# Optimization experiments

Hardware: AMD Instinct MI355X
Metric: run time of the kernel (lower is better)

## Reference

```python
import jax, jax.numpy as jnp
import numpy as np
from jax import lax


def _nextpow2(v):
    return int(np.ceil(np.log2(abs(v))))


def _dct_matrix(N):
    # Orthonormal DCT-II matrix C: dct(x, norm='ortho') along last axis == x @ C.T
    # C is orthogonal, so idct(y, norm='ortho') == y @ C.
    n = jnp.arange(N, dtype=jnp.float32)
    k = n[:, None]
    C = 2.0 * jnp.cos(jnp.pi * (2.0 * n[None, :] + 1.0) * k / (2.0 * N))
    s = jnp.where(jnp.arange(N) == 0,
                  1.0 / jnp.sqrt(4.0 * N),
                  1.0 / jnp.sqrt(2.0 * N)).astype(jnp.float32)
    return s[:, None] * C


def setup_inputs() -> dict:
    key = jax.random.key(0)
    x = jax.random.normal(key, (2, 1, 128, 128), dtype=jnp.float32)
    tau = jnp.asarray(7.7e-11, dtype=jnp.float32)
    chi = jnp.asarray(0.03, dtype=jnp.float32)
    return {"x": x, "tau": tau, "chi": chi}


def _forward(x, c0=1.0, sigma=1.0):
    B, _, Nz, Nx = x.shape
    Lx = 2 ** (_nextpow2(2 * Nx) + 1)  # padded width (512 for Nx=128)
    Ly = 2 ** (_nextpow2(2 * Nz) + 1)  # padded height (512 for Nz=128)
    Cy = _dct_matrix(Ly)
    Cx = Cy if Lx == Ly else _dct_matrix(Lx)

    # np.block([[Z, W, ZP_col], [Z, Z, ZP_col], [ZP_row]]) places W at rows 0:Nz, cols Nx:2Nx
    P = jnp.zeros((B, Ly, Lx), x.dtype).at[:, 0:Nz, Nx:2 * Nx].set(x[:, 0])

    # 2D orthonormal DCT-II: P_hat = Cy @ P @ Cx.T
    P_hat = jnp.einsum('ki,bij,lj->bkl', Cy, P, Cx)

    # Only row 0 of the 2D IDCT is kept per timestep; row-0 of the axis-0 IDCT is
    # a fixed weighted sum with weights a[k] = Cy[k, 0].
    a = Cy[:, 0]
    M = a[None, :, None] * P_hat  # (B, Ly, Lx)

    kx = jnp.arange(Lx, dtype=jnp.float32) / Lx * jnp.pi
    ky = jnp.arange(Ly, dtype=jnp.float32) / Ly * jnp.pi
    F = jnp.sqrt(ky[:, None] ** 2 + kx[None, :] ** 2)  # f.T in the source: (Ly, Lx)

    def step(carry, t):
        phase = jnp.cos(c0 * F * t)                 # (Ly, Lx), shared over batch
        return carry, jnp.einsum('kj,bkj->bj', phase, M)

    _, V = lax.scan(step, None, jnp.arange(Ly, dtype=jnp.float32))  # (T, B, Lx)

    # Remaining IDCT along the last axis, then /3
    Pdet = jnp.transpose(V @ Cx, (1, 0, 2)) / 3.0   # (B, T=Ly, Lx)

    # additive noise: N(0, sigma * std(Pdet)) per batch element (np.std -> ddof=0)
    std = jnp.std(Pdet, axis=(1, 2), keepdims=True)
    noise = jax.random.normal(jax.random.key(42), Pdet.shape, Pdet.dtype) * (sigma * std)
    return (Pdet + noise)[:, None]                  # (B, 1, Ly, Lx)


def reference(x, tau, chi):
    # tau, chi are module parameters but unused in the original forward path
    return _forward(x)
```

## Files before the change

kernel.cpp:

```cpp
#include <hip/hip_runtime.h>
#include <stdint.h>
#include <math.h>


#define HALF_N 262144
#define PI_F 3.14159274101257324f


__device__ __forceinline__ uint32_t rotl32(uint32_t v, int r) {
  return (v << r) | (v >> (32 - r));
}

__device__ __forceinline__ float erfinv_xla(float x) {
  float w = -log1pf(__fmul_rn(-x, x));
  float p;
  if (w < 5.0f) {
    w = w - 2.5f;
    p = 2.81022636e-08f;
    p = fmaf(p, w, 3.43273939e-07f);
    p = fmaf(p, w, -3.5233877e-06f);
    p = fmaf(p, w, -4.39150654e-06f);
    p = fmaf(p, w, 0.00021858087f);
    p = fmaf(p, w, -0.00125372503f);
    p = fmaf(p, w, -0.00417768164f);
    p = fmaf(p, w, 0.246640727f);
    p = fmaf(p, w, 1.50140941f);
  } else {
    w = __fsqrt_rn(w) - 3.0f;
    p = -0.000200214257f;
    p = fmaf(p, w, 0.000100950558f);
    p = fmaf(p, w, 0.00134934322f);
    p = fmaf(p, w, -0.00367342844f);
    p = fmaf(p, w, 0.00573950773f);
    p = fmaf(p, w, -0.0076224613f);
    p = fmaf(p, w, 0.00943887047f);
    p = fmaf(p, w, 1.00167406f);
    p = fmaf(p, w, 2.83297682f);
  }
  return p * x;
}

__device__ __forceinline__ float cy_elem(float n2p1, float kf, float sc) {
  float t1 = __fmul_rn(PI_F, n2p1);
  float arg = __fmul_rn(t1, kf) * (1.0f / 1024.0f);
  return __fmul_rn(sc, __fmul_rn(2.0f, __cosf(arg)));
}

__global__ __launch_bounds__(512, 4) void stageB_kernel(const float* __restrict__ x,
                                                        float* __restrict__ Vt) {
  __shared__ float cyl[128];
  __shared__ float us[256];
  __shared__ float4 kq[512];
  __shared__ float red[8][512];
  int j = blockIdx.x;
  int tid = threadIdx.x;
  float jf = (float)j;
  if (tid < 128) {
    float scj = (j == 0) ? (1.0f / __fsqrt_rn(2048.0f)) : 0.03125f;
    cyl[tid] = cy_elem((float)(2 * (128 + tid) + 1), jf, scj);
  }
  __syncthreads();
  if (tid < 256) {
    int b = tid >> 7, i = tid & 127;
    const float* xr = x + (b * 128 + i) * 128;
    float accA = 0.0f, accB = 0.0f;
    for (int jj = 0; jj < 128; jj += 8) {
      float4 xa = *(const float4*)&xr[jj];
      float4 xb = *(const float4*)&xr[jj + 4];
      float4 ca = *(const float4*)&cyl[jj];
      float4 cb = *(const float4*)&cyl[jj + 4];
      accA = fmaf(xa.x, ca.x, accA); accB = fmaf(xa.y, ca.y, accB);
      accA = fmaf(xa.z, ca.z, accA); accB = fmaf(xa.w, ca.w, accB);
      accA = fmaf(xb.x, cb.x, accA); accB = fmaf(xb.y, cb.y, accB);
      accA = fmaf(xb.z, cb.z, accA); accB = fmaf(xb.w, cb.w, accB);
    }
    us[tid] = accA + accB;
  }
  __syncthreads();
  {
    float kf = (float)tid;
    float sc = (tid == 0) ? (1.0f / __fsqrt_rn(2048.0f)) : 0.03125f;
    float a = cy_elem(1.0f, kf, sc);
    float acc0 = __fmul_rn(a, us[0]);
    float acc1 = __fmul_rn(a, us[128]);
    float accA0 = 0.f, accA1 = 0.f;
    {
      float c1 = cy_elem(3.0f, kf, sc);
      float c2 = cy_elem(5.0f, kf, sc);
      float c3 = cy_elem(7.0f, kf, sc);
      acc0 = fmaf(c1, us[1], acc0);   acc1 = fmaf(c1, us[129], acc1);
      accA0 = fmaf(c2, us[2], accA0); accA1 = fmaf(c2, us[130], accA1);
      acc0 = fmaf(c3, us[3], acc0);   acc1 = fmaf(c3, us[131], acc1);
    }
    for (int i = 4; i < 128; i += 4) {
      float b0 = (float)(2 * i + 1);
      float c0 = cy_elem(b0, kf, sc);
      float c1 = cy_elem(__fadd_rn(b0, 2.0f), kf, sc);
      float c2 = cy_elem(__fadd_rn(b0, 4.0f), kf, sc);
      float c3 = cy_elem(__fadd_rn(b0, 6.0f), kf, sc);
      float4 u0 = *(const float4*)&us[i];
      float4 u1 = *(const float4*)&us[128 + i];
      acc0 = fmaf(c0, u0.x, acc0);   acc1 = fmaf(c0, u1.x, acc1);
      accA0 = fmaf(c1, u0.y, accA0); accA1 = fmaf(c1, u1.y, accA1);
      acc0 = fmaf(c2, u0.z, acc0);   acc1 = fmaf(c2, u1.z, acc1);
      accA0 = fmaf(c3, u0.w, accA0); accA1 = fmaf(c3, u1.w, accA1);
    }
    acc0 += accA0;
    acc1 += accA1;
    const float w0 = PI_F / 512.0f;
    float ky = __fmul_rn(kf, w0);
    float kx = __fmul_rn(jf, w0);
    float fsv = __fsqrt_rn(__fadd_rn(__fmul_rn(ky, ky), __fmul_rn(kx, kx)));
    float cs = __cosf(__fmul_rn(fsv, 64.0f));
    kq[tid] = make_float4(fsv, __fmul_rn(a, acc0), __fmul_rn(a, acc1), cs);
  }
  __syncthreads();
  int kg = tid >> 6, tg = tid & 63;
  int kbeg = kg << 6;
  float tfa = (float)tg;
  float tfb = (float)(tg + 64);
  float a0[8], a1[8];
#pragma unroll
  for (int n = 0; n < 8; ++n) { a0[n] = 0.0f; a1[n] = 0.0f; }
  for (int kk = 0; kk < 64; ++kk) {
    float4 q = kq[kbeg + kk];
    float F = q.x, m0 = q.y, m1 = q.z;
    float k2 = q.w + q.w;
    float ca = __cosf(__fmul_rn(F, tfa));
    float cb = __cosf(__fmul_rn(F, tfb));
    a0[0] = fmaf(ca, m0, a0[0]); a1[0] = fmaf(ca, m1, a1[0]);
    a0[1] = fmaf(cb, m0, a0[1]); a1[1] = fmaf(cb, m1, a1[1]);
#pragma unroll
    for (int n = 2; n < 8; ++n) {
      float cn = fmaf(k2, cb, -ca);
      a0[n] = fmaf(cn, m0, a0[n]); a1[n] = fmaf(cn, m1, a1[n]);
      ca = cb; cb = cn;
    }
  }
#pragma unroll
  for (int n = 0; n < 8; ++n) red[kg][(n << 6) + tg] = a0[n];
  __syncthreads();
  float s0 = red[0][tid];
#pragma unroll
  for (int g = 1; g < 8; ++g) s0 += red[g][tid];
  __syncthreads();
#pragma unroll
  for (int n = 0; n < 8; ++n) red[kg][(n << 6) + tg] = a1[n];
  __syncthreads();
  float s1 = red[0][tid];
#pragma unroll
  for (int g = 1; g < 8; ++g) s1 += red[g][tid];
  Vt[(j << 10) + tid] = s0;
  Vt[(j << 10) + 512 + tid] = s1;
}

__global__ __launch_bounds__(256, 4) void stageC_kernel(const float* __restrict__ Vt,
                                                        float* __restrict__ out,
                                                        float* __restrict__ partial) {
  __shared__ float vq[1024];
  int t = blockIdx.x;
  int tid = threadIdx.x;
  {
    const float* b0p = Vt + (tid << 10);
    const float* b1p = b0p + 512;
    vq[2 * tid] = b0p[t];
    vq[2 * tid + 1] = b1p[t];
    const float* b0q = Vt + ((tid + 256) << 10);
    const float* b1q = b0q + 512;
    vq[2 * tid + 512] = b0q[t];
    vq[2 * tid + 513] = b1q[t];
  }
  __syncthreads();
  int l = tid;
  float t1 = __fmul_rn(PI_F, (float)(2 * l + 1));
  float cth = __cosf(__fmul_rn(t1, 1.0f) * (1.0f / 1024.0f));
  float k2 = cth + cth;
  float cy0 = __fmul_rn(1.0f / __fsqrt_rn(2048.0f), 2.0f);
  float c16 = __fmul_rn(cy0, 16.0f);
  float e0, e1, o0, o1;
  float c_m1, c_m2;
  {
    float2 v0 = *(const float2*)&vq[0];
    e0 = __fmul_rn(c16, v0.x);
    e1 = __fmul_rn(c16, v0.y);
    float2 v1 = *(const float2*)&vq[2];
    o0 = __fmul_rn(cth, v1.x);
    o1 = __fmul_rn(cth, v1.y);
    float c2v = __cosf(__fmul_rn(t1, 2.0f) * (1.0f / 1024.0f));
    float2 v2 = *(const float2*)&vq[4];
    e0 = fmaf(c2v, v2.x, e0); e1 = fmaf(c2v, v2.y, e1);
    c_m2 = cth; c_m1 = c2v;
#pragma unroll
    for (int j = 3; j < 16; ++j) {
      float cn = fmaf(k2, c_m1, -c_m2);
      float2 v = *(const float2*)&vq[j << 1];
      if (j & 1) { o0 = fmaf(cn, v.x, o0); o1 = fmaf(cn, v.y, o1); }
      else       { e0 = fmaf(cn, v.x, e0); e1 = fmaf(cn, v.y, e1); }
      c_m2 = c_m1; c_m1 = cn;
    }
  }
  for (int j0 = 16; j0 < 512; j0 += 16) {
    float jb = (float)j0;
    float ca = __cosf(__fmul_rn(t1, jb) * (1.0f / 1024.0f));
    float cb = __cosf(__fmul_rn(t1, __fadd_rn(jb, 1.0f)) * (1.0f / 1024.0f));
    float2 va = *(const float2*)&vq[j0 << 1];
    e0 = fmaf(ca, va.x, e0); e1 = fmaf(ca, va.y, e1);
    float2 vb = *(const float2*)&vq[(j0 + 1) << 1];
    o0 = fmaf(cb, vb.x, o0); o1 = fmaf(cb, vb.y, o1);
    c_m2 = ca; c_m1 = cb;
#pragma unroll
    for (int n = 2; n < 16; ++n) {
      float cn = fmaf(k2, c_m1, -c_m2);
      float2 v = *(const float2*)&vq[(j0 + n) << 1];
      if (n & 1) { o0 = fmaf(cn, v.x, o0); o1 = fmaf(cn, v.y, o1); }
      else       { e0 = fmaf(cn, v.x, e0); e1 = fmaf(cn, v.y, e1); }
      c_m2 = c_m1; c_m1 = cn;
    }
  }
  float pA0 = __fmul_rn(e0 + o0, 0.0625f) / 3.0f;
  float pA1 = __fmul_rn(e1 + o1, 0.0625f) / 3.0f;
  float pB0 = __fmul_rn(e0 - o0, 0.0625f) / 3.0f;
  float pB1 = __fmul_rn(e1 - o1, 0.0625f) / 3.0f;
  int lr = 511 - l;
  out[(t << 9) + l] = pA0;
  out[HALF_N + (t << 9) + l] = pA1;
  out[(t << 9) + lr] = pB0;
  out[HALF_N + (t << 9) + lr] = pB1;
  float s0 = pA0 + pB0, q0 = fmaf(pA0, pA0, pB0 * pB0);
  float s1 = pA1 + pB1, q1 = fmaf(pA1, pA1, pB1 * pB1);
  for (int off = 32; off > 0; off >>= 1) {
    s0 += __shfl_down(s0, off);
    q0 += __shfl_down(q0, off);
    s1 += __shfl_down(s1, off);
    q1 += __shfl_down(q1, off);
  }
  __shared__ float red[4][4];
  int wave = tid >> 6;
  if ((tid & 63) == 0) {
    red[wave][0] = s0; red[wave][1] = q0; red[wave][2] = s1; red[wave][3] = q1;
  }
  __syncthreads();
  if (tid == 0) {
    float a0 = 0.f, a1 = 0.f, a2 = 0.f, a3 = 0.f;
    for (int wv = 0; wv < 4; ++wv) {
      a0 += red[wv][0]; a1 += red[wv][1]; a2 += red[wv][2]; a3 += red[wv][3];
    }
    partial[blockIdx.x * 4 + 0] = a0;
    partial[blockIdx.x * 4 + 1] = a1;
    partial[blockIdx.x * 4 + 2] = a2;
    partial[blockIdx.x * 4 + 3] = a3;
  }
}

__global__ __launch_bounds__(256) void noise_kernel(float* __restrict__ out,
                                                    const float* __restrict__ partial) {
  int tid = threadIdx.x;
  const float4* pq = (const float4*)partial;
  float4 pa = pq[tid];
  float4 pb = pq[tid + 256];
  float s0 = pa.x + pb.x, q0 = pa.y + pb.y, s1 = pa.z + pb.z, q1 = pa.w + pb.w;
  for (int off = 32; off > 0; off >>= 1) {
    s0 += __shfl_down(s0, off);
    q0 += __shfl_down(q0, off);
    s1 += __shfl_down(s1, off);
    q1 += __shfl_down(q1, off);
  }
  __shared__ float red[4][4];
  int wave = tid >> 6;
  if ((tid & 63) == 0) {
    red[wave][0] = s0; red[wave][1] = q0; red[wave][2] = s1; red[wave][3] = q1;
  }
  __syncthreads();
  float S = red[0][0] + red[1][0] + red[2][0] + red[3][0];
  float Q = red[0][1] + red[1][1] + red[2][1] + red[3][1];
  float S2 = red[0][2] + red[1][2] + red[2][2] + red[3][2];
  float Q2 = red[0][3] + red[1][3] + red[2][3] + red[3][3];
  const float invN = 1.0f / 262144.0f;
  float m0 = S * invN, m1 = S2 * invN;
  float std0 = __fsqrt_rn(fmaxf(Q * invN - m0 * m0, 0.0f));
  float std1 = __fsqrt_rn(fmaxf(Q2 * invN - m1 * m1, 0.0f));

  int i = blockIdx.x * 256 + tid;
  uint32_t x0 = 0u;
  uint32_t x1 = (uint32_t)i;
  const uint32_t k0 = 0u, k1 = 42u;
  const uint32_t k2 = k0 ^ k1 ^ 0x1BD11BDAu;
  x0 += k0; x1 += k1;
#define QR(r) x0 += x1; x1 = rotl32(x1, r); x1 ^= x0;
  QR(13) QR(15) QR(26) QR(6)
  x0 += k1; x1 += k2 + 1u;
  QR(17) QR(29) QR(16) QR(24)
  x0 += k2; x1 += k0 + 2u;
  QR(13) QR(15) QR(26) QR(6)
  x0 += k0; x1 += k1 + 3u;
  QR(17) QR(29) QR(16) QR(24)
  x0 += k1; x1 += k2 + 4u;
  QR(13) QR(15) QR(26) QR(6)
  x0 += k2; x1 += k0 + 5u;
#undef QR
  uint32_t bits = x0 ^ x1;
  const float lo = __uint_as_float(0xBF7FFFFFu);
  float f = __uint_as_float((bits >> 9) | 0x3F800000u) - 1.0f;
  float u = fmaxf(lo, __fadd_rn(__fmul_rn(f, 2.0f), lo));
  const float sqrt2 = 1.41421356237309515f;
  out[i] += (i < HALF_N ? std0 : std1) * (sqrt2 * erfinv_xla(u));
}

extern "C" void kernel_launch(void* const* d_in, const int* in_sizes, int n_in,
                              void* d_out, int out_size, void* d_ws, size_t ws_size,
                              hipStream_t stream) {
  const float* x = (const float*)d_in[0];
  float* ws = (float*)d_ws;
  float* Vt      = ws;
  float* partial = ws + 524288;
  float* out = (float*)d_out;

  stageB_kernel<<<512, 512, 0, stream>>>(x, Vt);
  stageC_kernel<<<512, 256, 0, stream>>>(Vt, out, partial);
  noise_kernel<<<2048, 256, 0, stream>>>(out, partial);
}
```

Before: 102.7 us.

## Use Chebyshev recurrence for DCT coefficients and lengthen time recurrence chains

In the k-row DCT contraction, most cosine coefficients are now produced with the Chebyshev three-term recurrence. The seed is 2cos(pi*k/512), and exact cos evaluation is redone every 16 terms, so far fewer __cosf calls are needed. In the main phase loop, each thread now covers 32 k values instead of 64 and runs a 16-step recurrence instead of 8, with step 32 instead of 64, so fewer direct cosines are computed per output. This doubles the per-thread accumulator registers, doubles the shared reduction buffer to 16x512 floats, and lets error build up over longer recurrence chains.

Result: faster. 97.29 us (-5.3%).

```diff
diff --git a/kernel.cpp b/kernel.cpp
--- a/kernel.cpp
+++ b/kernel.cpp
@@ -51,7 +51,7 @@
   __shared__ float cyl[128];
   __shared__ float us[256];
   __shared__ float4 kq[512];
-  __shared__ float red[8][512];
+  __shared__ float red[16][512];
   int j = blockIdx.x;
   int tid = threadIdx.x;
   float jf = (float)j;
@@ -80,30 +80,62 @@
   {
     float kf = (float)tid;
     float sc = (tid == 0) ? (1.0f / __fsqrt_rn(2048.0f)) : 0.03125f;
+    float thc = __cosf(__fmul_rn(kf, PI_F / 512.0f));
+    float k2b = thc + thc;
     float a = cy_elem(1.0f, kf, sc);
+    float c1 = cy_elem(3.0f, kf, sc);
     float acc0 = __fmul_rn(a, us[0]);
     float acc1 = __fmul_rn(a, us[128]);
     float accA0 = 0.f, accA1 = 0.f;
-    {
-      float c1 = cy_elem(3.0f, kf, sc);
-      float c2 = cy_elem(5.0f, kf, sc);
-      float c3 = cy_elem(7.0f, kf, sc);
-      acc0 = fmaf(c1, us[1], acc0);   acc1 = fmaf(c1, us[129], acc1);
-      accA0 = fmaf(c2, us[2], accA0); accA1 = fmaf(c2, us[130], accA1);
-      acc0 = fmaf(c3, us[3], acc0);   acc1 = fmaf(c3, us[131], acc1);
-    }
-    for (int i = 4; i < 128; i += 4) {
-      float b0 = (float)(2 * i + 1);
-      float c0 = cy_elem(b0, kf, sc);
-      float c1 = cy_elem(__fadd_rn(b0, 2.0f), kf, sc);
-      float c2 = cy_elem(__fadd_rn(b0, 4.0f), kf, sc);
-      float c3 = cy_elem(__fadd_rn(b0, 6.0f), kf, sc);
-      float4 u0 = *(const float4*)&us[i];
-      float4 u1 = *(const float4*)&us[128 + i];
-      acc0 = fmaf(c0, u0.x, acc0);   acc1 = fmaf(c0, u1.x, acc1);
-      accA0 = fmaf(c1, u0.y, accA0); accA1 = fmaf(c1, u1.y, accA1);
-      acc0 = fmaf(c2, u0.z, acc0);   acc1 = fmaf(c2, u1.z, acc1);
-      accA0 = fmaf(c3, u0.w, accA0); accA1 = fmaf(c3, u1.w, accA1);
+    acc0 = fmaf(c1, us[1], acc0);   acc1 = fmaf(c1, us[129], acc1);
+    float cc2 = fmaf(k2b, c1, -a);
+    accA0 = fmaf(cc2, us[2], accA0); accA1 = fmaf(cc2, us[130], accA1);
+    float cc3 = fmaf(k2b, cc2, -c1);
+    acc0 = fmaf(cc3, us[3], acc0);   acc1 = fmaf(cc3, us[131], acc1);
+    float cm2 = cc2, cm1 = cc3;
+#pragma unroll
+    for (int q = 1; q < 4; ++q) {
+      int i = q << 2;
+      float4 v0 = *(const float4*)&us[i];
+      float4 v1 = *(const float4*)&us[128 + i];
+      float d0 = fmaf(k2b, cm1, -cm2);
+      acc0 = fmaf(d0, v0.x, acc0);   acc1 = fmaf(d0, v1.x, acc1);
+      float d1 = fmaf(k2b, d0, -cm1);
+      accA0 = fmaf(d1, v0.y, accA0); accA1 = fmaf(d1, v1.y, accA1);
+      float d2 = fmaf(k2b, d1, -d0);
+      acc0 = fmaf(d2, v0.z, acc0);   acc1 = fmaf(d2, v1.z, acc1);
+      float d3 = fmaf(k2b, d2, -d1);
+      accA0 = fmaf(d3, v0.w, accA0); accA1 = fmaf(d3, v1.w, accA1);
+      cm2 = d2; cm1 = d3;
+    }
+    for (int i0 = 16; i0 < 128; i0 += 16) {
+      float b0f = (float)(2 * i0 + 1);
+      float ca = cy_elem(b0f, kf, sc);
+      float cb = cy_elem(__fadd_rn(b0f, 2.0f), kf, sc);
+      float4 u0 = *(const float4*)&us[i0];
+      float4 u1 = *(const float4*)&us[128 + i0];
+      acc0 = fmaf(ca, u0.x, acc0);   acc1 = fmaf(ca, u1.x, acc1);
+      accA0 = fmaf(cb, u0.y, accA0); accA1 = fmaf(cb, u1.y, accA1);
+      float d2 = fmaf(k2b, cb, -ca);
+      acc0 = fmaf(d2, u0.z, acc0);   acc1 = fmaf(d2, u1.z, acc1);
+      float d3 = fmaf(k2b, d2, -cb);
+      accA0 = fmaf(d3, u0.w, accA0); accA1 = fmaf(d3, u1.w, accA1);
+      cm2 = d2; cm1 = d3;
+#pragma unroll
+      for (int q = 1; q < 4; ++q) {
+        int i = i0 + (q << 2);
+        float4 v0 = *(const float4*)&us[i];
+        float4 v1 = *(const float4*)&us[128 + i];
+        float d0 = fmaf(k2b, cm1, -cm2);
+        acc0 = fmaf(d0, v0.x, acc0);   acc1 = fmaf(d0, v1.x, acc1);
+        float d1 = fmaf(k2b, d0, -cm1);
+        accA0 = fmaf(d1, v0.y, accA0); accA1 = fmaf(d1, v1.y, accA1);
+        float e2 = fmaf(k2b, d1, -d0);
+        acc0 = fmaf(e2, v0.z, acc0);   acc1 = fmaf(e2, v1.z, acc1);
+        float e3 = fmaf(k2b, e2, -d1);
+        accA0 = fmaf(e3, v0.w, accA0); accA1 = fmaf(e3, v1.w, accA1);
+        cm2 = e2; cm1 = e3;
+      }
     }
     acc0 += accA0;
     acc1 += accA1;
@@ -111,18 +143,18 @@
     float ky = __fmul_rn(kf, w0);
     float kx = __fmul_rn(jf, w0);
     float fsv = __fsqrt_rn(__fadd_rn(__fmul_rn(ky, ky), __fmul_rn(kx, kx)));
-    float cs = __cosf(__fmul_rn(fsv, 64.0f));
+    float cs = __cosf(__fmul_rn(fsv, 32.0f));
     kq[tid] = make_float4(fsv, __fmul_rn(a, acc0), __fmul_rn(a, acc1), cs);
   }
   __syncthreads();
-  int kg = tid >> 6, tg = tid & 63;
-  int kbeg = kg << 6;
+  int kg = tid >> 5, tg = tid & 31;
+  int kbeg = kg << 5;
   float tfa = (float)tg;
-  float tfb = (float)(tg + 64);
-  float a0[8], a1[8];
-#pragma unroll
-  for (int n = 0; n < 8; ++n) { a0[n] = 0.0f; a1[n] = 0.0f; }
-  for (int kk = 0; kk < 64; ++kk) {
+  float tfb = (float)(tg + 32);
+  float a0[16], a1[16];
+#pragma unroll
+  for (int n = 0; n < 16; ++n) { a0[n] = 0.0f; a1[n] = 0.0f; }
+  for (int kk = 0; kk < 32; ++kk) {
     float4 q = kq[kbeg + kk];
     float F = q.x, m0 = q.y, m1 = q.z;
     float k2 = q.w + q.w;
@@ -131,25 +163,25 @@
     a0[0] = fmaf(ca, m0, a0[0]); a1[0] = fmaf(ca, m1, a1[0]);
     a0[1] = fmaf(cb, m0, a0[1]); a1[1] = fmaf(cb, m1, a1[1]);
 #pragma unroll
-    for (int n = 2; n < 8; ++n) {
+    for (int n = 2; n < 16; ++n) {
       float cn = fmaf(k2, cb, -ca);
       a0[n] = fmaf(cn, m0, a0[n]); a1[n] = fmaf(cn, m1, a1[n]);
       ca = cb; cb = cn;
     }
   }
 #pragma unroll
-  for (int n = 0; n < 8; ++n) red[kg][(n << 6) + tg] = a0[n];
+  for (int n = 0; n < 16; ++n) red[kg][(n << 5) + tg] = a0[n];
   __syncthreads();
   float s0 = red[0][tid];
 #pragma unroll
-  for (int g = 1; g < 8; ++g) s0 += red[g][tid];
-  __syncthreads();
-#pragma unroll
-  for (int n = 0; n < 8; ++n) red[kg][(n << 6) + tg] = a1[n];
+  for (int g = 1; g < 16; ++g) s0 += red[g][tid];
+  __syncthreads();
+#pragma unroll
+  for (int n = 0; n < 16; ++n) red[kg][(n << 5) + tg] = a1[n];
   __syncthreads();
   float s1 = red[0][tid];
 #pragma unroll
-  for (int g = 1; g < 8; ++g) s1 += red[g][tid];
+  for (int g = 1; g < 16; ++g) s1 += red[g][tid];
   Vt[(j << 10) + tid] = s0;
   Vt[(j << 10) + 512 + tid] = s1;
 }
```
